# Performance work log

Hardware: AMD Instinct MI355X
Metric: run time of the kernel (lower is better)

## Reference

```python
import jax, jax.numpy as jnp
import numpy as np

B = 131072
IN_DIM = 310   # 300 + zdimension_Gap(10)
H1 = 128       # g_neural_network_width
D = 100        # hard-coded data_t / generate_data width
SLOPE = 0.01   # torch LeakyReLU default negative_slope


def _leaky(v):
    return jnp.where(v >= 0, v, SLOPE * v)


def setup_inputs() -> dict:
    key = jax.random.key(0)
    ks = jax.random.split(key, 8)
    # kaiming_normal fan_in, a=0: std = sqrt(2 / fan_in)
    W1 = jax.random.normal(ks[0], (IN_DIM, 10), jnp.float32) * np.sqrt(2.0 / IN_DIM)
    b1 = jnp.zeros((10,), jnp.float32)
    W2 = jax.random.normal(ks[1], (10, H1), jnp.float32) * np.sqrt(2.0 / 10)
    b2 = jnp.zeros((H1,), jnp.float32)
    W3 = jax.random.normal(ks[2], (H1, 2), jnp.float32) * np.sqrt(2.0 / H1)
    b3 = jnp.zeros((2,), jnp.float32)
    x = jax.random.normal(ks[3], (B, IN_DIM), jnp.float32)
    data_t = jax.random.normal(ks[4], (B, D), jnp.float32)
    return {"x": x, "data_t": data_t, "W1": W1, "b1": b1,
            "W2": W2, "b2": b2, "W3": W3, "b3": b3}


def reference(x, data_t, W1, b1, W2, b2, W3, b3):
    # 3-layer MLP with LeakyReLU -> coeff [B, 2]
    h = _leaky(x @ W1 + b1)
    h = _leaky(h @ W2 + b2)
    coeff = _leaky(h @ W3 + b3)
    # polynomial basis: only power-1 (data_t) and power-2 (data_t**2) terms are used
    t2 = data_t * data_t  # [B, D]
    # generate_data[i] = coeff[i,0]*data_t[i] + coeff[i,1]*data_t[i]**2 (vectorized over batch)
    generate_data = coeff[:, 0:1] * data_t + coeff[:, 1:2] * t2
    return generate_data
```

## Files before the change

kernel.cpp:

```cpp
#include <hip/hip_runtime.h>
#include <stdint.h>

typedef float f32x2 __attribute__((ext_vector_type(2)));
typedef float f32x4 __attribute__((ext_vector_type(4)));

#define TILE_F 19840
#define NTPB   4
#define PSTR   162
#define CP_OFF 10368
#define CPSTR  34
#define H1_OFF 12544
#define H1STR  14
#define A_F    13440
#define APW    840
#define BPW    400
#define LDSF   (TILE_F + 128)
#define LDS_BYTES (LDSF * 4)

__device__ __forceinline__ float leaky(float v) { return fmaxf(v, 0.01f * v); }
__device__ __forceinline__ f32x2 leaky2(f32x2 v) {
    return __builtin_elementwise_max(v, v * 0.01f);
}

__device__ __forceinline__ void gload16(const float* g, float* l) {
    auto gp = reinterpret_cast<const float __attribute__((address_space(1)))*>(
        reinterpret_cast<uintptr_t>(g));
    auto lp = reinterpret_cast<float __attribute__((address_space(3)))*>(
        reinterpret_cast<uintptr_t>(l));
    __builtin_amdgcn_global_load_lds(gp, lp, 16, 0, 0);
}

__device__ __forceinline__ void stage_A(const float* src, float* dst, int lane) {
    #pragma unroll
    for (int i = 0; i < 3; ++i) gload16(src + i * 256, dst + i * 256);
    if (lane < 18) gload16(src + 768, dst + 768);
}
__device__ __forceinline__ void stage_B(const float* src, float* dst, int lane) {
    gload16(src, dst);
    if (lane < 36) gload16(src + 256, dst + 256);
}

template<int KQ>
__device__ __forceinline__ void fma_xk(const float* xk, const float* __restrict__ Wb,
                                       float* acc) {
    #pragma unroll
    for (int k = 0; k < KQ; ++k) {
        #pragma unroll
        for (int j = 0; j < 10; ++j)
            acc[j] = fmaf(xk[k], Wb[k * 10 + j], acc[j]);
    }
}

__global__ __launch_bounds__(1024, 8) void gen_mlp_r18(
    const float* __restrict__ x, const float* __restrict__ data_t,
    const float* __restrict__ W1, const float* __restrict__ b1,
    const float* __restrict__ W2, const float* __restrict__ b2,
    const float* __restrict__ W3, const float* __restrict__ b3,
    float* __restrict__ out)
{
    extern __shared__ float lds[];
    float* buf = lds;
    float* ccs = lds + TILE_F;

    const int t    = threadIdx.x;
    const int lane = t & 63;
    const int row  = lane;
    const int wq   = __builtin_amdgcn_readfirstlane(t >> 6);

    const int tile0 = blockIdx.x * NTPB;

    {
        const float* g = x + (size_t)tile0 * TILE_F;
        stage_A(g + wq * APW + lane * 4,       buf + wq * APW,       lane);
        stage_B(g + A_F + wq * BPW + lane * 4, buf + A_F + wq * BPW, lane);
    }
    asm volatile("s_waitcnt vmcnt(0)" ::: "memory");
    __builtin_amdgcn_s_barrier();

    #pragma unroll 1
    for (int it = 0; it < NTPB; ++it) {
        const int tile  = tile0 + it;
        const int tnext = (it + 1 < NTPB) ? tile + 1 : tile;
        const float* gnext = x + (size_t)tnext * TILE_F;

        const f32x4* dt4 = (const f32x4*)data_t + (size_t)tile * 1600;
        f32x4 tv0 = dt4[t], tv1;
        if (t < 576) tv1 = dt4[1024 + t];

        float xk[20];
        {
            const float* xr = buf + row * 310 + wq * 20;
            if (wq == 15) {
                #pragma unroll
                for (int q = 0; q < 5; ++q)
                    *(f32x2*)&xk[2 * q] = *(const f32x2*)(xr + 2 * q);
            } else {
                #pragma unroll
                for (int q = 0; q < 10; ++q)
                    *(f32x2*)&xk[2 * q] = *(const f32x2*)(xr + 2 * q);
            }
        }
        asm volatile("s_waitcnt lgkmcnt(0)" ::: "memory");
        __builtin_amdgcn_s_barrier();

        stage_B(gnext + A_F + wq * BPW + lane * 4, buf + A_F + wq * BPW, lane);

        float acc[10] = {0,0,0,0,0,0,0,0,0,0};
        if (wq == 15) fma_xk<10>(xk, W1 + 3000, acc);
        else          fma_xk<20>(xk, W1 + wq * 200, acc);

        {
            float* pw = buf + row * PSTR + wq * 10;
            #pragma unroll
            for (int j = 0; j < 5; ++j)
                *(f32x2*)(pw + 2 * j) = (f32x2){acc[2 * j], acc[2 * j + 1]};
        }
        asm volatile("s_waitcnt lgkmcnt(0)" ::: "memory");
        __builtin_amdgcn_s_barrier();

        if (wq < 10) {
            const float* pr = buf + row * PSTR + wq;
            float s = b1[wq];
            #pragma unroll
            for (int sl = 0; sl < 16; ++sl) s += pr[sl * 10];
            buf[H1_OFF + row * H1STR + wq] = leaky(s);
        }
        asm volatile("s_waitcnt lgkmcnt(0)" ::: "memory");
        __builtin_amdgcn_s_barrier();

        float h1[10];
        {
            const float* hr = buf + H1_OFF + row * H1STR;
            #pragma unroll
            for (int m = 0; m < 5; ++m) {
                f32x2 v = *(const f32x2*)(hr + 2 * m);
                h1[2 * m] = v.x; h1[2 * m + 1] = v.y;
            }
        }

        float hh[8];
        #pragma unroll
        for (int jj = 0; jj < 8; ++jj) hh[jj] = b2[wq * 8 + jj];
        #pragma unroll
        for (int k = 0; k < 10; ++k) {
            #pragma unroll
            for (int jj = 0; jj < 8; ++jj)
                hh[jj] = fmaf(h1[k], W2[k * 128 + wq * 8 + jj], hh[jj]);
        }
        f32x2 p = {0.f, 0.f};
        #pragma unroll
        for (int jj = 0; jj < 8; ++jj) {
            const float s = leaky(hh[jj]);
            p.x = fmaf(s, W3[(wq * 8 + jj) * 2 + 0], p.x);
            p.y = fmaf(s, W3[(wq * 8 + jj) * 2 + 1], p.y);
        }

        *(f32x2*)(buf + CP_OFF + row * CPSTR + 2 * wq) = p;
        asm volatile("s_waitcnt lgkmcnt(0)" ::: "memory");
        __builtin_amdgcn_s_barrier();

        if (wq == 0) {
            const float* cb = buf + CP_OFF + row * CPSTR;
            f32x2 q = {b3[0], b3[1]};
            #pragma unroll
            for (int i = 0; i < 16; ++i) {
                f32x2 v = *(const f32x2*)(cb + 2 * i);
                q.x += v.x;
                q.y += v.y;
            }
            *(f32x2*)(ccs + 2 * row) = leaky2(q);
        }
        asm volatile("s_waitcnt lgkmcnt(0)" ::: "memory");
        __builtin_amdgcn_s_barrier();

        stage_A(gnext + wq * APW + lane * 4, buf + wq * APW, lane);

        f32x4* o4 = (f32x4*)out + (size_t)tile * 1600;
        {
            f32x2 cc = *(const f32x2*)(ccs + 2 * (t / 25));
            o4[t] = tv0 * (tv0 * cc.y + cc.x);
        }
        if (t < 576) {
            const int idx = 1024 + t;
            f32x2 cc = *(const f32x2*)(ccs + 2 * (idx / 25));
            o4[idx] = tv1 * (tv1 * cc.y + cc.x);
        }

        asm volatile("s_waitcnt vmcnt(1)" ::: "memory");
        __builtin_amdgcn_s_barrier();
    }
}

extern "C" void kernel_launch(void* const* d_in, const int* in_sizes, int n_in,
                              void* d_out, int out_size, void* d_ws, size_t ws_size,
                              hipStream_t stream) {
    const float* x      = (const float*)d_in[0];
    const float* data_t = (const float*)d_in[1];
    const float* W1     = (const float*)d_in[2];
    const float* b1     = (const float*)d_in[3];
    const float* W2     = (const float*)d_in[4];
    const float* b2     = (const float*)d_in[5];
    const float* W3     = (const float*)d_in[6];
    const float* b3     = (const float*)d_in[7];
    float* out = (float*)d_out;

    hipFuncSetAttribute((const void*)gen_mlp_r18,
                        hipFuncAttributeMaxDynamicSharedMemorySize, LDS_BYTES);
    gen_mlp_r18<<<512, 1024, LDS_BYTES, stream>>>(x, data_t, W1, b1, W2, b2, W3, b3, out);
}
```

Measured before the change: 51.87 us.

## Halve tile to 32 rows with 512-thread blocks and split-K within each wave

Shrinks each tile from 64 to 32 rows and launches 1024 blocks of 512 threads instead of 512 blocks of 1024. Each wave now covers 40 input columns, and its two half-waves each reduce 20 of them, combined with a cross-lane shuffle. The layer-2/3 work per wave doubles to 16 hidden units, and the staging and reduction layouts are resized to fit. The aim is smaller LDS per block, so more blocks fit per CU with finer load balancing, at the cost of extra shuffles and reworked async-load wait counts.

```diff
diff --git a/kernel.cpp b/kernel.cpp
--- a/kernel.cpp
+++ b/kernel.cpp
@@ -4,17 +4,18 @@
 typedef float f32x2 __attribute__((ext_vector_type(2)));
 typedef float f32x4 __attribute__((ext_vector_type(4)));
 
-#define TILE_F 19840
+#define ROWS   32
+#define TILE_F (ROWS * 310)
 #define NTPB   4
-#define PSTR   162
-#define CP_OFF 10368
-#define CPSTR  34
-#define H1_OFF 12544
+#define PSTR   82
+#define CP_OFF (ROWS * PSTR)
+#define CPSTR  18
+#define H1_OFF 3200
 #define H1STR  14
-#define A_F    13440
-#define APW    840
-#define BPW    400
-#define LDSF   (TILE_F + 128)
+#define A_F    3840
+#define APW    480
+#define BPW    760
+#define LDSF   (TILE_F + 64)
 #define LDS_BYTES (LDSF * 4)
 
 __device__ __forceinline__ float leaky(float v) { return fmaxf(v, 0.01f * v); }
@@ -31,27 +32,16 @@
 }
 
 __device__ __forceinline__ void stage_A(const float* src, float* dst, int lane) {
-    #pragma unroll
-    for (int i = 0; i < 3; ++i) gload16(src + i * 256, dst + i * 256);
-    if (lane < 18) gload16(src + 768, dst + 768);
+    gload16(src, dst);
+    if (lane < 56) gload16(src + 256, dst + 256);
 }
 __device__ __forceinline__ void stage_B(const float* src, float* dst, int lane) {
     gload16(src, dst);
-    if (lane < 36) gload16(src + 256, dst + 256);
-}
-
-template<int KQ>
-__device__ __forceinline__ void fma_xk(const float* xk, const float* __restrict__ Wb,
-                                       float* acc) {
-    #pragma unroll
-    for (int k = 0; k < KQ; ++k) {
-        #pragma unroll
-        for (int j = 0; j < 10; ++j)
-            acc[j] = fmaf(xk[k], Wb[k * 10 + j], acc[j]);
-    }
-}
-
-__global__ __launch_bounds__(1024, 8) void gen_mlp_r18(
+    gload16(src + 256, dst + 256);
+    if (lane < 62) gload16(src + 512, dst + 512);
+}
+
+__global__ __launch_bounds__(512, 8) void gen_mlp_r19(
     const float* __restrict__ x, const float* __restrict__ data_t,
     const float* __restrict__ W1, const float* __restrict__ b1,
     const float* __restrict__ W2, const float* __restrict__ b2,
@@ -62,10 +52,11 @@
     float* buf = lds;
     float* ccs = lds + TILE_F;
 
-    const int t    = threadIdx.x;
-    const int lane = t & 63;
-    const int row  = lane;
-    const int wq   = __builtin_amdgcn_readfirstlane(t >> 6);
+    const int t     = threadIdx.x;
+    const int lane  = t & 63;
+    const int row   = lane & 31;
+    const int kh    = lane >> 5;
+    const int wq    = __builtin_amdgcn_readfirstlane(t >> 6);
 
     const int tile0 = blockIdx.x * NTPB;
 
@@ -83,14 +74,16 @@
         const int tnext = (it + 1 < NTPB) ? tile + 1 : tile;
         const float* gnext = x + (size_t)tnext * TILE_F;
 
-        const f32x4* dt4 = (const f32x4*)data_t + (size_t)tile * 1600;
+        const f32x4* dt4 = (const f32x4*)data_t + (size_t)tile * (ROWS * 25);
         f32x4 tv0 = dt4[t], tv1;
-        if (t < 576) tv1 = dt4[1024 + t];
+        if (t < 288) tv1 = dt4[512 + t];
 
         float xk[20];
-        {
-            const float* xr = buf + row * 310 + wq * 20;
-            if (wq == 15) {
+        int nk = 20;
+        {
+            const float* xr = buf + row * 310 + wq * 40 + kh * 20;
+            if (wq == 7 && kh == 1) {
+                nk = 10;
                 #pragma unroll
                 for (int q = 0; q < 5; ++q)
                     *(f32x2*)&xk[2 * q] = *(const f32x2*)(xr + 2 * q);
@@ -106,10 +99,27 @@
         stage_B(gnext + A_F + wq * BPW + lane * 4, buf + A_F + wq * BPW, lane);
 
         float acc[10] = {0,0,0,0,0,0,0,0,0,0};
-        if (wq == 15) fma_xk<10>(xk, W1 + 3000, acc);
-        else          fma_xk<20>(xk, W1 + wq * 200, acc);
-
-        {
+        {
+            const float* Wb = W1 + (wq * 40 + kh * 20) * 10;
+            if (wq == 7 && kh == 1) {
+                #pragma unroll
+                for (int k = 0; k < 10; ++k)
+                    #pragma unroll
+                    for (int j = 0; j < 10; ++j)
+                        acc[j] = fmaf(xk[k], Wb[k * 10 + j], acc[j]);
+            } else {
+                #pragma unroll
+                for (int k = 0; k < 20; ++k)
+                    #pragma unroll
+                    for (int j = 0; j < 10; ++j)
+                        acc[j] = fmaf(xk[k], Wb[k * 10 + j], acc[j]);
+            }
+        }
+        #pragma unroll
+        for (int j = 0; j < 10; ++j)
+            acc[j] += __shfl_xor(acc[j], 32, 64);
+
+        if (kh == 0) {
             float* pw = buf + row * PSTR + wq * 10;
             #pragma unroll
             for (int j = 0; j < 5; ++j)
@@ -118,12 +128,13 @@
         asm volatile("s_waitcnt lgkmcnt(0)" ::: "memory");
         __builtin_amdgcn_s_barrier();
 
-        if (wq < 10) {
-            const float* pr = buf + row * PSTR + wq;
-            float s = b1[wq];
-            #pragma unroll
-            for (int sl = 0; sl < 16; ++sl) s += pr[sl * 10];
-            buf[H1_OFF + row * H1STR + wq] = leaky(s);
+        if (t < 320) {
+            const int hr = t / 10, hj = t - 10 * hr;
+            const float* pr = buf + hr * PSTR + hj;
+            float s = b1[hj];
+            #pragma unroll
+            for (int sl = 0; sl < 8; ++sl) s += pr[sl * 10];
+            buf[H1_OFF + hr * H1STR + hj] = leaky(s);
         }
         asm volatile("s_waitcnt lgkmcnt(0)" ::: "memory");
         __builtin_amdgcn_s_barrier();
@@ -138,32 +149,33 @@
             }
         }
 
-        float hh[8];
-        #pragma unroll
-        for (int jj = 0; jj < 8; ++jj) hh[jj] = b2[wq * 8 + jj];
+        float hh[16];
+        #pragma unroll
+        for (int jj = 0; jj < 16; ++jj) hh[jj] = b2[wq * 16 + jj];
         #pragma unroll
         for (int k = 0; k < 10; ++k) {
             #pragma unroll
-            for (int jj = 0; jj < 8; ++jj)
-                hh[jj] = fmaf(h1[k], W2[k * 128 + wq * 8 + jj], hh[jj]);
+            for (int jj = 0; jj < 16; ++jj)
+                hh[jj] = fmaf(h1[k], W2[k * 128 + wq * 16 + jj], hh[jj]);
         }
         f32x2 p = {0.f, 0.f};
         #pragma unroll
-        for (int jj = 0; jj < 8; ++jj) {
+        for (int jj = 0; jj < 16; ++jj) {
             const float s = leaky(hh[jj]);
-            p.x = fmaf(s, W3[(wq * 8 + jj) * 2 + 0], p.x);
-            p.y = fmaf(s, W3[(wq * 8 + jj) * 2 + 1], p.y);
-        }
-
-        *(f32x2*)(buf + CP_OFF + row * CPSTR + 2 * wq) = p;
-        asm volatile("s_waitcnt lgkmcnt(0)" ::: "memory");
-        __builtin_amdgcn_s_barrier();
-
-        if (wq == 0) {
+            p.x = fmaf(s, W3[(wq * 16 + jj) * 2 + 0], p.x);
+            p.y = fmaf(s, W3[(wq * 16 + jj) * 2 + 1], p.y);
+        }
+
+        if (kh == 0)
+            *(f32x2*)(buf + CP_OFF + row * CPSTR + 2 * wq) = p;
+        asm volatile("s_waitcnt lgkmcnt(0)" ::: "memory");
+        __builtin_amdgcn_s_barrier();
+
+        if (wq == 0 && kh == 0) {
             const float* cb = buf + CP_OFF + row * CPSTR;
             f32x2 q = {b3[0], b3[1]};
             #pragma unroll
-            for (int i = 0; i < 16; ++i) {
+            for (int i = 0; i < 8; ++i) {
                 f32x2 v = *(const f32x2*)(cb + 2 * i);
                 q.x += v.x;
                 q.y += v.y;
@@ -175,18 +187,18 @@
 
         stage_A(gnext + wq * APW + lane * 4, buf + wq * APW, lane);
 
-        f32x4* o4 = (f32x4*)out + (size_t)tile * 1600;
+        f32x4* o4 = (f32x4*)out + (size_t)tile * (ROWS * 25);
         {
             f32x2 cc = *(const f32x2*)(ccs + 2 * (t / 25));
             o4[t] = tv0 * (tv0 * cc.y + cc.x);
         }
-        if (t < 576) {
-            const int idx = 1024 + t;
+        if (t < 288) {
+            const int idx = 512 + t;
             f32x2 cc = *(const f32x2*)(ccs + 2 * (idx / 25));
             o4[idx] = tv1 * (tv1 * cc.y + cc.x);
         }
 
-        asm volatile("s_waitcnt vmcnt(1)" ::: "memory");
+        asm volatile("s_waitcnt vmcnt(2)" ::: "memory");
         __builtin_amdgcn_s_barrier();
     }
 }
@@ -204,7 +216,7 @@
     const float* b3     = (const float*)d_in[7];
     float* out = (float*)d_out;
 
-    hipFuncSetAttribute((const void*)gen_mlp_r18,
+    hipFuncSetAttribute((const void*)gen_mlp_r19,
                         hipFuncAttributeMaxDynamicSharedMemorySize, LDS_BYTES);
-    gen_mlp_r18<<<512, 1024, LDS_BYTES, stream>>>(x, data_t, W1, b1, W2, b2, W3, b3, out);
-}
+    gen_mlp_r19<<<1024, 512, LDS_BYTES, stream>>>(x, data_t, W1, b1, W2, b2, W3, b3, out);
+}
```

Measured after the change: 153.6 us. +196.2%, slower.
